# Performance work log

Measured on AMD Instinct MI355X. Metric: run time of the kernel, lower is better.

The kernel has to match this reference:

```python
import jax, jax.numpy as jnp
from jax import lax
import numpy as np

D_MODEL = 512
D_STATE = 16
D_CONV = 4
EXPAND = 2
D_INNER = EXPAND * D_MODEL  # 1024
DT_RANK = (D_MODEL + 15) // 16  # 32
FF_DIM = 1024
N_LAYERS = 2
B, L = 2, 2048


def setup_inputs() -> dict:
    key = jax.random.key(0)
    ks = jax.random.split(key, 16)
    s = 0.02
    x = jax.random.normal(ks[0], (B, L, D_MODEL), jnp.float32)
    in_proj_w = jax.random.normal(ks[1], (N_LAYERS, 2 * D_INNER, D_MODEL), jnp.float32) * s
    conv_w = jax.random.normal(ks[2], (N_LAYERS, D_INNER, D_CONV), jnp.float32) * 0.3
    conv_b = jax.random.normal(ks[3], (N_LAYERS, D_INNER), jnp.float32) * s
    x_proj_w = jax.random.normal(ks[4], (N_LAYERS, DT_RANK + 2 * D_STATE, D_INNER), jnp.float32) * s
    dt_proj_w = jax.random.normal(ks[5], (N_LAYERS, D_INNER, DT_RANK), jnp.float32) * s
    dt_proj_b = jax.random.normal(ks[6], (N_LAYERS, D_INNER), jnp.float32) * 0.5 - 4.0
    A_log = jnp.log(jnp.broadcast_to(jnp.arange(1, D_STATE + 1, dtype=jnp.float32), (N_LAYERS, D_INNER, D_STATE)))
    Dp = jnp.ones((N_LAYERS, D_INNER), jnp.float32)
    out_proj_w = jax.random.normal(ks[7], (N_LAYERS, D_MODEL, D_INNER), jnp.float32) * s
    mlp_w1 = jax.random.normal(ks[8], (FF_DIM, D_MODEL), jnp.float32) * s
    mlp_b1 = jnp.zeros((FF_DIM,), jnp.float32)
    mlp_w2 = jax.random.normal(ks[9], (D_MODEL, FF_DIM), jnp.float32) * s
    mlp_b2 = jnp.zeros((D_MODEL,), jnp.float32)
    return dict(x=x, in_proj_w=in_proj_w, conv_w=conv_w, conv_b=conv_b,
                x_proj_w=x_proj_w, dt_proj_w=dt_proj_w, dt_proj_b=dt_proj_b,
                A_log=A_log, Dp=Dp, out_proj_w=out_proj_w,
                mlp_w1=mlp_w1, mlp_b1=mlp_b1, mlp_w2=mlp_w2, mlp_b2=mlp_b2)


def _mamba_layer(x, ipw, cw, cb, xpw, dpw, dpb, Al, Dv, opw):
    # x: [B, L, d_model]
    b, l, _ = x.shape
    xz = jnp.einsum('bld,ed->ble', x, ipw)           # [B, L, 2*d_inner]
    xin, z = jnp.split(xz, 2, axis=-1)
    # causal depthwise conv1d (pad left d_conv-1)
    xc = jnp.transpose(xin, (0, 2, 1))               # [B, d_inner, L]
    xc = lax.conv_general_dilated(xc, cw[:, None, :], (1,), [(D_CONV - 1, 0)],
                                  feature_group_count=D_INNER)
    xin = jax.nn.silu(jnp.transpose(xc + cb[:, None], (0, 2, 1)))  # [B, L, d_inner]
    dbl = jnp.einsum('bld,ed->ble', xin, xpw)        # [B, L, dt_rank + 2*d_state]
    dt, Bm, Cm = jnp.split(dbl, [DT_RANK, DT_RANK + D_STATE], axis=-1)
    dt = jax.nn.softplus(jnp.einsum('blr,dr->bld', dt, dpw) + dpb)  # [B, L, d_inner]
    A = -jnp.exp(Al)                                  # [d_inner, d_state]
    dA = jnp.exp(dt[..., None] * A)                   # [B, L, d_inner, d_state]
    dBu = dt[..., None] * Bm[:, :, None, :] * xin[..., None]

    def step(h, inp):
        dA_t, dBu_t = inp
        h = dA_t * h + dBu_t
        return h, h

    h0 = jnp.zeros((b, D_INNER, D_STATE), x.dtype)
    _, hs = lax.scan(step, h0, (jnp.moveaxis(dA, 1, 0), jnp.moveaxis(dBu, 1, 0)))
    hs = jnp.moveaxis(hs, 0, 1)                       # [B, L, d_inner, d_state]
    y = jnp.einsum('blds,bls->bld', hs, Cm) + xin * Dv
    y = y * jax.nn.silu(z)
    return jnp.einsum('ble,de->bld', y, opw)


def reference(x, in_proj_w, conv_w, conv_b, x_proj_w, dt_proj_w, dt_proj_b,
              A_log, Dp, out_proj_w, mlp_w1, mlp_b1, mlp_w2, mlp_b2):
    residual = x
    for i in range(N_LAYERS):
        x = _mamba_layer(x, in_proj_w[i], conv_w[i], conv_b[i], x_proj_w[i],
                         dt_proj_w[i], dt_proj_b[i], A_log[i], Dp[i], out_proj_w[i])
    h = x + residual
    h = jax.nn.relu(jnp.einsum('bld,fd->blf', h, mlp_w1) + mlp_b1)  # dropout is identity in eval
    return jnp.einsum('blf,df->bld', h, mlp_w2) + mlp_b2
```

## Files before the change

kernel.cpp:

```cpp
#include <hip/hip_runtime.h>
#include <hip/hip_bf16.h>

#define BB 2
#define LL 2048
#define DMODEL 512
#define DSTATE 16
#define DINNER 1024
#define DTRANK 32
#define FFDIM 1024
#define MTOT (BB*LL)
#define SCL 64
#define NCC 32

typedef unsigned short u16;
typedef __attribute__((ext_vector_type(8))) short bf16x8;
typedef __attribute__((ext_vector_type(4))) float f32x4;

__device__ __forceinline__ float b2f(u16 u){
  unsigned v = ((unsigned)u) << 16; float f; __builtin_memcpy(&f, &v, 4); return f;
}
__device__ __forceinline__ u16 f2b(float f){
  unsigned u; __builtin_memcpy(&u, &f, 4);
  unsigned r = (u + 0x7FFFu + ((u >> 16) & 1u)) >> 16;
  return (u16)r;
}
__device__ __forceinline__ float siluf(float x){ return x / (1.f + __expf(-x)); }
__device__ __forceinline__ float softplusf(float v){
  return fmaxf(v, 0.f) + __logf(1.f + __expf(-fabsf(v)));
}

__device__ __forceinline__ float ldin(const void* p, size_t i, int bf){
  if (bf) return b2f(((const u16*)p)[i]);
  return ((const float*)p)[i];
}
__device__ __forceinline__ void stout(void* p, size_t i, int bf, float v){
  if (bf) ((u16*)p)[i] = f2b(v);
  else    ((float*)p)[i] = v;
}

__device__ __forceinline__ int getbf(const void* dp){
  return (*(const unsigned*)dp == 0x3F803F80u) ? 1 : 0;
}

template<int CVT>
__device__ __forceinline__ bf16x8 ld8(const void* P, size_t gi, int bf){
  if (!CVT || bf) return *(const bf16x8*)((const u16*)P + gi);
  float4 f0 = *(const float4*)((const float*)P + gi);
  float4 f1 = *(const float4*)((const float*)P + gi + 4);
  union { u16 u[8]; bf16x8 v; } t;
  t.u[0]=f2b(f0.x); t.u[1]=f2b(f0.y); t.u[2]=f2b(f0.z); t.u[3]=f2b(f0.w);
  t.u[4]=f2b(f1.x); t.u[5]=f2b(f1.y); t.u[6]=f2b(f1.z); t.u[7]=f2b(f1.w);
  return t.v;
}

#define CVT_IPW (2*2*DINNER*DMODEL)
#define CVT_XPW (2*64*DINNER)
#define CVT_DPW (2*DINNER*DTRANK)
#define CVT_OPW (2*DMODEL*DINNER)
#define CVT_W1  (FFDIM*DMODEL)
#define CVT_W2  (DMODEL*FFDIM)
#define CVT_CW  (2*DINNER*4)
#define CVT_CB  (2*DINNER)
#define CVT_TOT (CVT_IPW+CVT_XPW+CVT_DPW+CVT_OPW+CVT_W1+CVT_W2+CVT_CW+CVT_CB)
__global__ __launch_bounds__(256) void cvt_all_k(
    const void* __restrict__ ipw, const void* __restrict__ xpw,
    const void* __restrict__ dpw, const void* __restrict__ opw,
    const void* __restrict__ w1, const void* __restrict__ w2,
    const void* __restrict__ cw, const void* __restrict__ cb,
    u16* __restrict__ dst, const void* __restrict__ dprobe)
{
  const int bf = getbf(dprobe);
  size_t i4 = ((size_t)blockIdx.x * 256 + threadIdx.x) * 4;
  if (i4 >= CVT_TOT) return;
  const void* src; size_t off = i4;
  if      (off < CVT_IPW)                     { src = ipw; }
  else if ((off -= CVT_IPW) < CVT_XPW)        { src = xpw; }
  else if ((off -= CVT_XPW) < CVT_DPW)        { src = dpw; }
  else if ((off -= CVT_DPW) < CVT_OPW)        { src = opw; }
  else if ((off -= CVT_OPW) < CVT_W1)         { src = w1; }
  else if ((off -= CVT_W1)  < CVT_W2)         { src = w2; }
  else if ((off -= CVT_W2)  < CVT_CW)         { src = cw; }
  else     { off -= CVT_CW;                     src = cb; }
  ushort4 o;
  if (bf) {
    o = *(const ushort4*)((const u16*)src + off);
  } else {
    float4 f = *(const float4*)((const float*)src + off);
    o.x = f2b(f.x); o.y = f2b(f.y); o.z = f2b(f.z); o.w = f2b(f.w);
  }
  *(ushort4*)(dst + i4) = o;
}

template<int ACT, int CVA, int CVW, int CIN, int BM, int BN, int KB, int RESID>
__global__ __launch_bounds__(256) void gemm_mfma(
    const void* __restrict__ A, size_t aoff, int lda,
    const void* __restrict__ W, size_t woff,
    const void* __restrict__ bias, size_t boff,
    void* __restrict__ C, size_t coff, int ldc, int K,
    const void* __restrict__ xres, size_t xroff,
    const void* __restrict__ dprobe)
{
  const int bf = getbf(dprobe);
  constexpr int C8  = KB / 8;
  constexpr int TR  = 256 / C8;
  constexpr int ALD = BM / TR;
  constexpr int WLD = BN / TR;
  __shared__ __align__(16) u16 As[2][BM * KB];
  __shared__ __align__(16) u16 Ws[2][BN * KB];
  const int tid = threadIdx.x;
  const int row0 = blockIdx.y * BM, col0 = blockIdx.x * BN;
  const int wave = tid >> 6, lane = tid & 63;
  const int l15 = lane & 15, quad = lane >> 4;
  constexpr int WMT = (BM == 64) ? 1 : ((BN == 128) ? 4 : 2);
  const int mbase = (BM == 64) ? (wave * 16)
                  : ((BN == 128) ? (wave & 1) * 64 : wave * 32);
  const int nbase = (BM == 128 && BN == 128) ? (wave >> 1) * 64 : 0;

  const int rT = tid / C8, csw = tid % C8;
  const int scg = (KB == 32) ? (csw ^ ((rT >> 1) & 3)) : (csw ^ (rT & 7));
  const int lws = tid * 8;
  const size_t ab0 = aoff + (size_t)(row0 + rT) * lda + scg * 8;
  const size_t wb0 = woff + (size_t)(col0 + rT) * K   + scg * 8;

  f32x4 acc[WMT][4];
#pragma unroll
  for (int i = 0; i < WMT; i++)
#pragma unroll
    for (int j = 0; j < 4; j++) acc[i][j] = (f32x4){0.f,0.f,0.f,0.f};

  const int NT = K / KB;

  auto fchunk = [&](int r_, int g){
    return (KB == 32) ? (g ^ ((r_ >> 1) & 3)) : (g ^ (r_ & 7));
  };
  auto compute = [&](int cur_){
#pragma unroll
    for (int ks = 0; ks < KB / 32; ks++) {
      bf16x8 af_[WMT], bf_[4];
#pragma unroll
      for (int mt = 0; mt < WMT; mt++) {
        int r_ = mbase + mt * 16 + l15;
        af_[mt] = *(const bf16x8*)&As[cur_][r_ * KB + fchunk(r_, ks * 4 + quad) * 8];
      }
#pragma unroll
      for (int nt = 0; nt < 4; nt++) {
        int r_ = nbase + nt * 16 + l15;
        bf_[nt] = *(const bf16x8*)&Ws[cur_][r_ * KB + fchunk(r_, ks * 4 + quad) * 8];
      }
#pragma unroll
      for (int mt = 0; mt < WMT; mt++)
#pragma unroll
        for (int nt = 0; nt < 4; nt++)
          acc[mt][nt] = __builtin_amdgcn_mfma_f32_16x16x32_bf16(af_[mt], bf_[nt], acc[mt][nt], 0, 0, 0);
    }
  };

  bf16x8 ra0[ALD], rw0[WLD], ra1[ALD], rw1[WLD], ra2[ALD], rw2[WLD];

#define GLOAD(RA, RW, T) do { const int k1_ = (T) * KB;                        \
  _Pragma("unroll") for (int i = 0; i < ALD; i++)                              \
    RA[i] = ld8<CVA>(A, ab0 + k1_ + (size_t)i * TR * lda, bf);                 \
  _Pragma("unroll") for (int i = 0; i < WLD; i++)                              \
    RW[i] = ld8<CVW>(W, wb0 + k1_ + (size_t)i * TR * K, bf); } while (0)

#define GSTEP(RA, RW, T) do {                                                  \
  const int cur_ = (T) & 1;                                                    \
  _Pragma("unroll") for (int i = 0; i < ALD; i++)                              \
    *(bf16x8*)&As[cur_][lws + i * 2048] = RA[i];                               \
  _Pragma("unroll") for (int i = 0; i < WLD; i++)                              \
    *(bf16x8*)&Ws[cur_][lws + i * 2048] = RW[i];                               \
  if ((T) + 3 < NT) GLOAD(RA, RW, (T) + 3);                                    \
  __syncthreads();                                                             \
  compute(cur_);                                                               \
} while (0)

  GLOAD(ra0, rw0, 0);
  if (NT > 1) GLOAD(ra1, rw1, 1);
  if (NT > 2) GLOAD(ra2, rw2, 2);
  int t = 0;
  for (; t + 2 < NT; t += 3) {
    GSTEP(ra0, rw0, t);
    GSTEP(ra1, rw1, t + 1);
    GSTEP(ra2, rw2, t + 2);
  }
  if (t < NT)     GSTEP(ra0, rw0, t);
  if (t + 1 < NT) GSTEP(ra1, rw1, t + 1);
#undef GLOAD
#undef GSTEP

#pragma unroll
  for (int nt = 0; nt < 4; nt++) {
    int c = col0 + nbase + nt * 16 + l15;
    float bv = bias ? ldin(bias, boff + c, bf) : 0.f;
#pragma unroll
    for (int mt = 0; mt < WMT; mt++) {
      int rb = row0 + mbase + mt * 16 + quad * 4;
#pragma unroll
      for (int r = 0; r < 4; r++) {
        float v = acc[mt][nt][r] + bv;
        if (ACT == 1) v = softplusf(v);
        if (ACT == 2) v = fmaxf(v, 0.f);
        size_t ci = (size_t)(rb + r) * ldc + c;
        if (RESID) v += ldin(xres, xroff + ci, bf);
        if (CIN) stout(C, coff + ci, bf, v);
        else     ((u16*)C)[coff + ci] = f2b(v);
      }
    }
  }
}

template<int FST>
__global__ __launch_bounds__(256) void conv_k(
    const u16* __restrict__ xz, const void* __restrict__ cw, size_t cwo,
    const void* __restrict__ cb, size_t cbo, u16* __restrict__ xc,
    const void* __restrict__ dprobe)
{
  if (FST) {
    const u16* cw16 = (const u16*)cw;
    const u16* cb16 = (const u16*)cb;
    int idx8 = (blockIdx.x * 256 + threadIdx.x) * 8;
    int d8 = idx8 & 1023;
    int row = idx8 >> 10;
    int lb = row & (LL - 1);
    bf16x8 cwv0 = *(const bf16x8*)&cw16[cwo + d8*4];
    bf16x8 cwv1 = *(const bf16x8*)&cw16[cwo + d8*4 + 8];
    bf16x8 cwv2 = *(const bf16x8*)&cw16[cwo + d8*4 + 16];
    bf16x8 cwv3 = *(const bf16x8*)&cw16[cwo + d8*4 + 24];
    bf16x8 cbv  = *(const bf16x8*)&cb16[cbo + d8];
    bf16x8 xv0 = (bf16x8){0,0,0,0,0,0,0,0}, xv1 = xv0, xv2 = xv0, xv3 = xv0;
    if (lb >= 3) xv0 = *(const bf16x8*)&xz[(size_t)(row - 3) * 2048 + d8];
    if (lb >= 2) xv1 = *(const bf16x8*)&xz[(size_t)(row - 2) * 2048 + d8];
    if (lb >= 1) xv2 = *(const bf16x8*)&xz[(size_t)(row - 1) * 2048 + d8];
    xv3 = *(const bf16x8*)&xz[(size_t)row * 2048 + d8];
    bf16x8 ov;
#pragma unroll
    for (int i = 0; i < 8; i++) {
      float acc = b2f((u16)cbv[i]);
      int c0 = i * 4;
      float w0 = b2f((u16)((c0 < 8) ? cwv0[c0 & 7] : (c0 < 16) ? cwv1[c0 & 7] : (c0 < 24) ? cwv2[c0 & 7] : cwv3[c0 & 7]));
      float w1_ = b2f((u16)(((c0+1) < 8) ? cwv0[(c0+1) & 7] : ((c0+1) < 16) ? cwv1[(c0+1) & 7] : ((c0+1) < 24) ? cwv2[(c0+1) & 7] : cwv3[(c0+1) & 7]));
      float w2_ = b2f((u16)(((c0+2) < 8) ? cwv0[(c0+2) & 7] : ((c0+2) < 16) ? cwv1[(c0+2) & 7] : ((c0+2) < 24) ? cwv2[(c0+2) & 7] : cwv3[(c0+2) & 7]));
      float w3_ = b2f((u16)(((c0+3) < 8) ? cwv0[(c0+3) & 7] : ((c0+3) < 16) ? cwv1[(c0+3) & 7] : ((c0+3) < 24) ? cwv2[(c0+3) & 7] : cwv3[(c0+3) & 7]));
      acc += w0 * b2f((u16)xv0[i]);
      acc += w1_ * b2f((u16)xv1[i]);
      acc += w2_ * b2f((u16)xv2[i]);
      acc += w3_ * b2f((u16)xv3[i]);
      ov[i] = (short)f2b(siluf(acc));
    }
    *(bf16x8*)&xc[idx8] = ov;
  } else {
    const int bf = getbf(dprobe);
    int idx = blockIdx.x * 256 + threadIdx.x;
    int d = idx & 1023;
    int row = idx >> 10;
    int lb = row & (LL - 1);
    float acc = ldin(cb, cbo + d, bf);
#pragma unroll
    for (int k = 0; k < 4; k++) {
      int lk = lb - 3 + k;
      if (lk >= 0) acc += ldin(cw, cwo + d*4 + k, bf) * b2f(xz[(size_t)(row - 3 + k) * 2048 + d]);
    }
    xc[idx] = f2b(siluf(acc));
  }
}

template<int CVW>
__global__ __launch_bounds__(256) void scan_A_k(
    const u16* __restrict__ xc,
    const u16* __restrict__ dbl,
    const void* __restrict__ dpwp, size_t dpwo,
    const void* __restrict__ dpbp, size_t dpbo,
    const void* __restrict__ Alog, size_t alo,
    float* __restrict__ Pc, float* __restrict__ Sc,
    const void* __restrict__ dprobe)
{
  const int bf = getbf(dprobe);
  int bid = blockIdx.x;
  int b = bid >> 9;
  int c = (bid >> 4) & (NCC - 1);
  int g = bid & 15;
  int t = threadIdx.x;
  int dl = t >> 2, sq = t & 3;
  int d0 = g * 64, d = d0 + dl;
  int rowb = b * LL + c * SCL;

  __shared__ __align__(16) u16 dts[64 * 64];
  __shared__ __align__(16) u16 us[64 * 64];
  __shared__ __align__(16) float Bs[64 * 20];
  u16* dbls = dts;
  u16* dpws = dts + 64 * 32;

  {
    int r = t >> 2, c8 = (t & 3) * 8;
    *(bf16x8*)&dbls[r * 32 + c8] =
        *(const bf16x8*)&dbl[(size_t)(rowb + r) * 64 + c8];
    *(bf16x8*)&dpws[r * 32 + c8] =
        ld8<CVW>(dpwp, dpwo + (size_t)(d0 + r) * DTRANK + c8, bf);
  }
#pragma unroll
  for (int p = 0; p < 2; p++) {
    int seg = p * 256 + t;
    int r = seg >> 3, c8 = (seg & 7) * 8;
    bf16x8 uv = *(const bf16x8*)&xc[(size_t)(rowb + r) * 1024 + d0 + c8];
    int coff = r >> 3, roff = r & 7;
#pragma unroll
    for (int i = 0; i < 8; i++) {
      int dd = c8 + i;
      us[dd * 64 + ((coff ^ (dd & 7)) << 3) + roff] = (u16)uv[i];
    }
  }
  if (t < 128) {
    int l = t >> 1, grp = t & 1;
    bf16x8 v = *(const bf16x8*)&dbl[(size_t)(rowb + l) * 64 + 32 + grp * 8];
    f32x4 f0 = {b2f((u16)v[0]), b2f((u16)v[1]), b2f((u16)v[2]), b2f((u16)v[3])};
    f32x4 f1 = {b2f((u16)v[4]), b2f((u16)v[5]), b2f((u16)v[6]), b2f((u16)v[7])};
    *(f32x4*)&Bs[l * 20 + grp * 8]     = f0;
    *(f32x4*)&Bs[l * 20 + grp * 8 + 4] = f1;
  }
  float Av[4];
#pragma unroll
  for (int j = 0; j < 4; j++)
    Av[j] = -__expf(ldin(Alog, alo + (size_t)d * DSTATE + sq * 4 + j, bf));
  __syncthreads();

  {
    int wv = t >> 6, lane = t & 63;
    int fl = lane & 15, qd = lane >> 4;
    bf16x8 afr  = *(const bf16x8*)&dbls[(wv * 16 + fl) * 32 + qd * 8];
    bf16x8 bfr0 = *(const bf16x8*)&dpws[(fl)      * 32 + qd * 8];
    bf16x8 bfr1 = *(const bf16x8*)&dpws[(16 + fl) * 32 + qd * 8];
    bf16x8 bfr2 = *(const bf16x8*)&dpws[(32 + fl) * 32 + qd * 8];
    bf16x8 bfr3 = *(const bf16x8*)&dpws[(48 + fl) * 32 + qd * 8];
    __syncthreads();
    f32x4 zz = {0.f, 0.f, 0.f, 0.f};
    f32x4 a0 = __builtin_amdgcn_mfma_f32_16x16x32_bf16(afr, bfr0, zz, 0, 0, 0);
    f32x4 a1 = __builtin_amdgcn_mfma_f32_16x16x32_bf16(afr, bfr1, zz, 0, 0, 0);
    f32x4 a2 = __builtin_amdgcn_mfma_f32_16x16x32_bf16(afr, bfr2, zz, 0, 0, 0);
    f32x4 a3 = __builtin_amdgcn_mfma_f32_16x16x32_bf16(afr, bfr3, zz, 0, 0, 0);
    int lc = wv * 2 + (qd >> 1);
    int off = (qd & 1) * 4;
#define DTWR(AN, NT) do {                                                      \
    int dd_ = (NT) * 16 + fl;                                                  \
    float bvv_ = ldin(dpbp, dpbo + d0 + dd_, bf);                              \
    ushort4 pk_;                                                               \
    pk_.x = f2b(softplusf(AN[0] + bvv_));                                      \
    pk_.y = f2b(softplusf(AN[1] + bvv_));                                      \
    pk_.z = f2b(softplusf(AN[2] + bvv_));                                      \
    pk_.w = f2b(softplusf(AN[3] + bvv_));                                      \
    *(ushort4*)&dts[dd_ * 64 + ((lc ^ (dd_ & 7)) << 3) + off] = pk_; } while (0)
    DTWR(a0, 0); DTWR(a1, 1); DTWR(a2, 2); DTWR(a3, 3);
#undef DTWR
  }
  __syncthreads();

  float h[4] = {0.f,0.f,0.f,0.f}, P[4] = {1.f,1.f,1.f,1.f};
  for (int cc = 0; cc < 8; cc++) {
    int base = dl * 64 + ((cc ^ (dl & 7)) << 3);
    bf16x8 dt8 = *(const bf16x8*)&dts[base];
    bf16x8 u8  = *(const bf16x8*)&us[base];
#pragma unroll
    for (int i = 0; i < 8; i++) {
      int l = cc * 8 + i;
      float dtv = b2f((u16)dt8[i]);
      float uv  = b2f((u16)u8[i]);
      float dtu = dtv * uv;
      f32x4 B4 = *(const f32x4*)&Bs[l * 20 + sq * 4];
#pragma unroll
      for (int j = 0; j < 4; j++) {
        float dA = __expf(dtv * Av[j]);
        h[j] = dA * h[j] + dtu * B4[j];
        P[j] *= dA;
      }
    }
  }
  size_t o = (((size_t)b * DINNER + d) * NCC + c) * DSTATE + sq * 4;
  *(f32x4*)&Pc[o] = (f32x4){P[0], P[1], P[2], P[3]};
  *(f32x4*)&Sc[o] = (f32x4){h[0], h[1], h[2], h[3]};
}

__global__ __launch_bounds__(256) void scan_B_k(
    float* __restrict__ Pc, const float* __restrict__ Sc)
{
  int idx = blockIdx.x * 256 + threadIdx.x;
  int bd = idx >> 4, s = idx & 15;
  float h = 0.f;
  for (int c = 0; c < NCC; c++) {
    size_t o = ((size_t)bd * NCC + c) * DSTATE + s;
    float P = Pc[o], S = Sc[o];
    Pc[o] = h;
    h = P * h + S;
  }
}

template<int CVW>
__global__ __launch_bounds__(256) void scan_C_k(
    u16* __restrict__ dtp, int sdt, const u16* __restrict__ xz,
    const u16* __restrict__ xc,
    const u16* __restrict__ dbl,
    const void* __restrict__ dpwp, size_t dpwo,
    const void* __restrict__ dpbp, size_t dpbo,
    const void* __restrict__ Alog, size_t alo,
    const void* __restrict__ Dpt, size_t dpo, const float* __restrict__ Hinit,
    const void* __restrict__ dprobe)
{
  const int bf = getbf(dprobe);
  int bid = blockIdx.x;
  int b = bid >> 9;
  int c = (bid >> 4) & (NCC - 1);
  int g = bid & 15;
  int t = threadIdx.x;
  int dl = t >> 2, sq = t & 3;
  int d0 = g * 64, d = d0 + dl;
  int rowb = b * LL + c * SCL;

  __shared__ __align__(16) u16 dts[64 * 64];
  __shared__ __align__(16) u16 us[64 * 64];
  __shared__ __align__(16) u16 outs[64 * 64];
  __shared__ __align__(16) float BCs[64 * 36];
  u16* dbls = dts;
  u16* dpws = dts + 64 * 32;

  {
    int r = t >> 2, c8 = (t & 3) * 8;
    *(bf16x8*)&dbls[r * 32 + c8] =
        *(const bf16x8*)&dbl[(size_t)(rowb + r) * 64 + c8];
    *(bf16x8*)&dpws[r * 32 + c8] =
        ld8<CVW>(dpwp, dpwo + (size_t)(d0 + r) * DTRANK + c8, bf);
  }
#pragma unroll
  for (int p = 0; p < 2; p++) {
    int seg = p * 256 + t;
    int r = seg >> 3, c8 = (seg & 7) * 8;
    bf16x8 uv = *(const bf16x8*)&xc[(size_t)(rowb + r) * 1024 + d0 + c8];
    int coff = r >> 3, roff = r & 7;
#pragma unroll
    for (int i = 0; i < 8; i++) {
      int dd = c8 + i;
      us[dd * 64 + ((coff ^ (dd & 7)) << 3) + roff] = (u16)uv[i];
    }
  }
  {
    int l = t >> 2, grp = t & 3;
    bf16x8 v = *(const bf16x8*)&dbl[(size_t)(rowb + l) * 64 + 32 + grp * 8];
    f32x4 f0 = {b2f((u16)v[0]), b2f((u16)v[1]), b2f((u16)v[2]), b2f((u16)v[3])};
    f32x4 f1 = {b2f((u16)v[4]), b2f((u16)v[5]), b2f((u16)v[6]), b2f((u16)v[7])};
    *(f32x4*)&BCs[l * 36 + grp * 8]     = f0;
    *(f32x4*)&BCs[l * 36 + grp * 8 + 4] = f1;
  }
  float Av[4];
#pragma unroll
  for (int j = 0; j < 4; j++)
    Av[j] = -__expf(ldin(Alog, alo + (size_t)d * DSTATE + sq * 4 + j, bf));
  float Dv = ldin(Dpt, dpo + d, bf);
  float h[4];
  size_t o = (((size_t)b * DINNER + d) * NCC + c) * DSTATE + sq * 4;
  f32x4 h4 = *(const f32x4*)&Hinit[o];
  h[0] = h4[0]; h[1] = h4[1]; h[2] = h4[2]; h[3] = h4[3];
  __syncthreads();

  {
    int wv = t >> 6, lane = t & 63;
    int fl = lane & 15, qd = lane >> 4;
    bf16x8 afr  = *(const bf16x8*)&dbls[(wv * 16 + fl) * 32 + qd * 8];
    bf16x8 bfr0 = *(const bf16x8*)&dpws[(fl)      * 32 + qd * 8];
    bf16x8 bfr1 = *(const bf16x8*)&dpws[(16 + fl) * 32 + qd * 8];
    bf16x8 bfr2 = *(const bf16x8*)&dpws[(32 + fl) * 32 + qd * 8];
    bf16x8 bfr3 = *(const bf16x8*)&dpws[(48 + fl) * 32 + qd * 8];
    __syncthreads();
    f32x4 zz = {0.f, 0.f, 0.f, 0.f};
    f32x4 a0 = __builtin_amdgcn_mfma_f32_16x16x32_bf16(afr, bfr0, zz, 0, 0, 0);
    f32x4 a1 = __builtin_amdgcn_mfma_f32_16x16x32_bf16(afr, bfr1, zz, 0, 0, 0);
    f32x4 a2 = __builtin_amdgcn_mfma_f32_16x16x32_bf16(afr, bfr2, zz, 0, 0, 0);
    f32x4 a3 = __builtin_amdgcn_mfma_f32_16x16x32_bf16(afr, bfr3, zz, 0, 0, 0);
    int lc = wv * 2 + (qd >> 1);
    int off = (qd & 1) * 4;
#define DTWR(AN, NT) do {                                                      \
    int dd_ = (NT) * 16 + fl;                                                  \
    float bvv_ = ldin(dpbp, dpbo + d0 + dd_, bf);                              \
    ushort4 pk_;                                                               \
    pk_.x = f2b(softplusf(AN[0] + bvv_));                                      \
    pk_.y = f2b(softplusf(AN[1] + bvv_));                                      \
    pk_.z = f2b(softplusf(AN[2] + bvv_));                                      \
    pk_.w = f2b(softplusf(AN[3] + bvv_));                                      \
    *(ushort4*)&dts[dd_ * 64 + ((lc ^ (dd_ & 7)) << 3) + off] = pk_; } while (0)
    DTWR(a0, 0); DTWR(a1, 1); DTWR(a2, 2); DTWR(a3, 3);
#undef DTWR
  }
  __syncthreads();

  for (int cc = 0; cc < 8; cc++) {
    int base = dl * 64 + ((cc ^ (dl & 7)) << 3);
    bf16x8 dt8 = *(const bf16x8*)&dts[base];
    bf16x8 u8  = *(const bf16x8*)&us[base];
#pragma unroll
    for (int i = 0; i < 8; i++) {
      int l = cc * 8 + i;
      float dtv = b2f((u16)dt8[i]);
      float uv  = b2f((u16)u8[i]);
      float dtu = dtv * uv;
      f32x4 B4 = *(const f32x4*)&BCs[l * 36 + sq * 4];
      f32x4 C4 = *(const f32x4*)&BCs[l * 36 + 16 + sq * 4];
      float y = 0.f;
#pragma unroll
      for (int j = 0; j < 4; j++) {
        float dA = __expf(dtv * Av[j]);
        h[j] = dA * h[j] + dtu * B4[j];
        y += h[j] * C4[j];
      }
      y += __shfl_xor(y, 1);
      y += __shfl_xor(y, 2);
      if (sq == 0) outs[l * 64 + dl] = f2b(y + uv * Dv);
    }
  }
  __syncthreads();
#pragma unroll
  for (int p = 0; p < 2; p++) {
    int seg = p * 256 + t;
    int r = seg >> 3, c8 = (seg & 7) * 8;
    bf16x8 yv = *(const bf16x8*)&outs[r * 64 + c8];
    bf16x8 zv = *(const bf16x8*)&xz[(size_t)(rowb + r) * 2048 + 1024 + d0 + c8];
    bf16x8 ov;
#pragma unroll
    for (int i = 0; i < 8; i++) {
      float z = b2f((u16)zv[i]);
      ov[i] = (short)f2b(b2f((u16)yv[i]) * siluf(z));
    }
    *(bf16x8*)&dtp[(size_t)(rowb + r) * sdt + d0 + c8] = ov;
  }
}

extern "C" void kernel_launch(void* const* d_in, const int* in_sizes, int n_in,
                              void* d_out, int out_size, void* d_ws, size_t ws_size,
                              hipStream_t stream) {
  const void* x_in = d_in[0];
  const void* ipw  = d_in[1];
  const void* cw   = d_in[2];
  const void* cb   = d_in[3];
  const void* xpw  = d_in[4];
  const void* dpw  = d_in[5];
  const void* dpb  = d_in[6];
  const void* Alog = d_in[7];
  const void* Dpt  = d_in[8];
  const void* opw  = d_in[9];
  const void* w1   = d_in[10];
  const void* b1   = d_in[11];
  const void* w2   = d_in[12];
  const void* b2   = d_in[13];

  const bool full = ws_size >= (size_t)64 * 1024 * 1024;
  const bool bfh = (in_sizes[1] == (int)(CVT_IPW * 2));

  if (full) {
    float* Pc = (float*)((char*)d_ws + 64);
    float* Sc = Pc + (size_t)BB*DINNER*NCC*DSTATE;
    u16* p = (u16*)(Sc + (size_t)BB*DINNER*NCC*DSTATE);
    u16* cvt0  = p;
    u16* ipw16 = p;  p += (size_t)CVT_IPW;
    u16* xpw16 = p;  p += (size_t)CVT_XPW;
    u16* dpw16 = p;  p += (size_t)CVT_DPW;
    u16* opw16 = p;  p += (size_t)CVT_OPW;
    u16* w116  = p;  p += (size_t)CVT_W1;
    u16* w216  = p;  p += (size_t)CVT_W2;
    u16* cw16  = p;  p += (size_t)CVT_CW;
    u16* cb16  = p;  p += (size_t)CVT_CB;
    u16* xz    = p;  p += (size_t)MTOT*2*DINNER;
    u16* xc    = p;  p += (size_t)MTOT*DINNER;
    u16* dty   = p;  p += (size_t)MTOT*DINNER;
    u16* dbl   = p;
    u16* bx = xc;
    u16* resid = xz;
    u16* hid = xz + (size_t)4*1024*1024;

    const u16* Wipw = bfh ? (const u16*)ipw : ipw16;
    const u16* Wxpw = bfh ? (const u16*)xpw : xpw16;
    const u16* Wdpw = bfh ? (const u16*)dpw : dpw16;
    const u16* Wopw = bfh ? (const u16*)opw : opw16;
    const u16* Ww1  = bfh ? (const u16*)w1  : w116;
    const u16* Ww2  = bfh ? (const u16*)w2  : w216;
    const u16* Wcw  = bfh ? (const u16*)cw  : cw16;
    const u16* Wcb  = bfh ? (const u16*)cb  : cb16;
    if (!bfh)
      cvt_all_k<<<(CVT_TOT/4 + 255)/256, 256, 0, stream>>>(
          ipw, xpw, dpw, opw, w1, w2, cw, cb, cvt0, Dpt);

    for (int layer = 0; layer < 2; layer++) {
      size_t ipw_o = (size_t)layer*2*DINNER*DMODEL;
      size_t cw_o  = (size_t)layer*DINNER*4,  cb_o = (size_t)layer*DINNER;
      size_t xpw_o = (size_t)layer*64*DINNER, dpw_o = (size_t)layer*DINNER*DTRANK;
      size_t dpb_o = (size_t)layer*DINNER,    al_o = (size_t)layer*DINNER*DSTATE;
      size_t dp_o  = (size_t)layer*DINNER,    opw_o = (size_t)layer*DMODEL*DINNER;
      if (layer == 0)
        gemm_mfma<0,1,0,0,128,128,32,0><<<dim3(16, 32), 256, 0, stream>>>(
            x_in, 0, DMODEL, Wipw, ipw_o, nullptr, 0, xz, 0, 2048, DMODEL,
            nullptr, 0, Dpt);
      else
        gemm_mfma<0,0,0,0,128,128,32,0><<<dim3(16, 32), 256, 0, stream>>>(
            bx, 0, DMODEL, Wipw, ipw_o, nullptr, 0, xz, 0, 2048, DMODEL,
            nullptr, 0, Dpt);
      conv_k<1><<<MTOT*DINNER/2048, 256, 0, stream>>>(
          xz, Wcw, cw_o, Wcb, cb_o, xc, Dpt);
      gemm_mfma<0,0,0,0,64,64,32,0><<<dim3(1, 64), 256, 0, stream>>>(
          xc, 0, DINNER, Wxpw, xpw_o, nullptr, 0, dbl, 0, 64, DINNER,
          nullptr, 0, Dpt);
      scan_A_k<0><<<BB*NCC*16, 256, 0, stream>>>(
          xc, dbl, Wdpw, dpw_o, dpb, dpb_o, Alog, al_o, Pc, Sc, Dpt);
      scan_B_k<<<BB*64, 256, 0, stream>>>(Pc, Sc);
      scan_C_k<0><<<BB*NCC*16, 256, 0, stream>>>(
          dty, 1024, xz, xc, dbl, Wdpw, dpw_o, dpb, dpb_o, Alog, al_o,
          Dpt, dp_o, Pc, Dpt);
      if (layer == 0)
        gemm_mfma<0,0,0,0,64,64,32,0><<<dim3(8, 64), 256, 0, stream>>>(
            dty, 0, 1024, Wopw, opw_o, nullptr, 0, bx, 0, DMODEL, DINNER,
            nullptr, 0, Dpt);
      else
        gemm_mfma<0,0,0,0,64,64,32,1><<<dim3(8, 64), 256, 0, stream>>>(
            dty, 0, 1024, Wopw, opw_o, nullptr, 0, resid, 0, DMODEL, DINNER,
            x_in, 0, Dpt);
    }
    gemm_mfma<2,0,0,0,64,64,32,0><<<dim3(16, 64), 256, 0, stream>>>(
        resid, 0, DMODEL, Ww1, 0, b1, 0, hid, 0, FFDIM, DMODEL,
        nullptr, 0, Dpt);
    gemm_mfma<0,0,0,1,64,64,32,0><<<dim3(8, 64), 256, 0, stream>>>(
        hid, 0, FFDIM, Ww2, 0, b2, 0, d_out, 0, DMODEL, FFDIM,
        nullptr, 0, Dpt);
  } else {
    float* Pc = (float*)((char*)d_ws + 64);
    float* Sc = Pc + (size_t)DINNER*NCC*DSTATE;
    u16* p = (u16*)(Sc + (size_t)DINNER*NCC*DSTATE);
    u16* xz  = p;  p += (size_t)LL*2*DINNER;
    u16* xc  = p;  p += (size_t)LL*DINNER;
    u16* bxF = p;  p += (size_t)MTOT*DMODEL;
    u16* dbl = p;
    u16* hid = xz + (size_t)2*1024*1024;

    for (int layer = 0; layer < 2; layer++) {
      size_t ipw_o = (size_t)layer*2*DINNER*DMODEL;
      size_t cw_o  = (size_t)layer*DINNER*4,  cb_o = (size_t)layer*DINNER;
      size_t xpw_o = (size_t)layer*64*DINNER, dpw_o = (size_t)layer*DINNER*DTRANK;
      size_t dpb_o = (size_t)layer*DINNER,    al_o = (size_t)layer*DINNER*DSTATE;
      size_t dp_o  = (size_t)layer*DINNER,    opw_o = (size_t)layer*DMODEL*DINNER;
      for (int b = 0; b < BB; b++) {
        size_t ro = (size_t)b * LL * DMODEL;
        if (layer == 0)
          gemm_mfma<0,1,1,0,128,128,32,0><<<dim3(16, 16), 256, 0, stream>>>(
              x_in, ro, DMODEL, ipw, ipw_o, nullptr, 0, xz, 0, 2048, DMODEL,
              nullptr, 0, Dpt);
        else
          gemm_mfma<0,0,1,0,128,128,32,0><<<dim3(16, 16), 256, 0, stream>>>(
              bxF, ro, DMODEL, ipw, ipw_o, nullptr, 0, xz, 0, 2048, DMODEL,
              nullptr, 0, Dpt);
        conv_k<0><<<LL*DINNER/256, 256, 0, stream>>>(xz, cw, cw_o, cb, cb_o, xc, Dpt);
        gemm_mfma<0,0,1,0,64,64,32,0><<<dim3(1, 32), 256, 0, stream>>>(
            xc, 0, DINNER, xpw, xpw_o, nullptr, 0, dbl, 0, 64, DINNER,
            nullptr, 0, Dpt);
        scan_A_k<1><<<NCC*16, 256, 0, stream>>>(
            xc, dbl, dpw, dpw_o, dpb, dpb_o, Alog, al_o, Pc, Sc, Dpt);
        scan_B_k<<<64, 256, 0, stream>>>(Pc, Sc);
        scan_C_k<1><<<NCC*16, 256, 0, stream>>>(
            xz, 2048, xz, xc, dbl, dpw, dpw_o, dpb, dpb_o, Alog, al_o,
            Dpt, dp_o, Pc, Dpt);
        if (layer == 0)
          gemm_mfma<0,0,1,0,64,64,32,0><<<dim3(8, 32), 256, 0, stream>>>(
              xz, 0, 2048, opw, opw_o, nullptr, 0, bxF, ro, DMODEL, DINNER,
              nullptr, 0, Dpt);
        else
          gemm_mfma<0,0,1,0,64,64,32,1><<<dim3(8, 32), 256, 0, stream>>>(
              xz, 0, 2048, opw, opw_o, nullptr, 0, bxF, ro, DMODEL, DINNER,
              x_in, ro, Dpt);
      }
    }
    for (int b = 0; b < BB; b++) {
      size_t ro = (size_t)b * LL * DMODEL;
      gemm_mfma<2,0,1,0,64,64,32,0><<<dim3(16, 32), 256, 0, stream>>>(
          bxF, ro, DMODEL, w1, 0, b1, 0, hid, 0, FFDIM, DMODEL,
          nullptr, 0, Dpt);
      gemm_mfma<0,0,1,1,64,64,32,0><<<dim3(8, 32), 256, 0, stream>>>(
          hid, 0, FFDIM, w2, 0, b2, 0, d_out, ro, DMODEL, FFDIM,
          nullptr, 0, Dpt);
    }
  }
}
```

Measured before the change: 331.9 us.

## Fuse chunked scan passes into one cooperative kernel with grid syncs

Replaces the three scan launches (chunk-local scan, cross-chunk prefix, and output pass) with one cooperative kernel that uses two grid-wide syncs. The delta and u tiles stay in shared memory across the passes, so the second pass no longer reloads them or recomputes the dt projection. It also removes two kernel launches. The cost is that all 1024 blocks must be co-resident at 4 blocks per CU under the launch bounds, and two grid barriers are added. If the cooperative launch fails, the code falls back to the old three kernels.

```diff
diff --git a/kernel.cpp b/kernel.cpp
--- a/kernel.cpp
+++ b/kernel.cpp
@@ -1,5 +1,8 @@
 #include <hip/hip_runtime.h>
 #include <hip/hip_bf16.h>
+#include <hip/hip_cooperative_groups.h>
+
+namespace cg = cooperative_groups;
 
 #define BB 2
 #define LL 2048
@@ -264,13 +267,13 @@
   }
 }
 
-template<int CVW>
-__global__ __launch_bounds__(256) void scan_A_k(
-    const u16* __restrict__ xc,
-    const u16* __restrict__ dbl,
+__global__ __launch_bounds__(256, 4) void scan_fused_k(
+    u16* __restrict__ dtp, int sdt, const u16* __restrict__ xz,
+    const u16* __restrict__ xc, const u16* __restrict__ dbl,
     const void* __restrict__ dpwp, size_t dpwo,
     const void* __restrict__ dpbp, size_t dpbo,
     const void* __restrict__ Alog, size_t alo,
+    const void* __restrict__ Dpt, size_t dpo,
     float* __restrict__ Pc, float* __restrict__ Sc,
     const void* __restrict__ dprobe)
 {
@@ -286,7 +289,8 @@
 
   __shared__ __align__(16) u16 dts[64 * 64];
   __shared__ __align__(16) u16 us[64 * 64];
-  __shared__ __align__(16) float Bs[64 * 20];
+  __shared__ __align__(16) u16 outs[64 * 64];
+  __shared__ __align__(16) float BCs[64 * 36];
   u16* dbls = dts;
   u16* dpws = dts + 64 * 32;
 
@@ -295,7 +299,7 @@
     *(bf16x8*)&dbls[r * 32 + c8] =
         *(const bf16x8*)&dbl[(size_t)(rowb + r) * 64 + c8];
     *(bf16x8*)&dpws[r * 32 + c8] =
-        ld8<CVW>(dpwp, dpwo + (size_t)(d0 + r) * DTRANK + c8, bf);
+        ld8<0>(dpwp, dpwo + (size_t)(d0 + r) * DTRANK + c8, bf);
   }
 #pragma unroll
   for (int p = 0; p < 2; p++) {
@@ -309,18 +313,19 @@
       us[dd * 64 + ((coff ^ (dd & 7)) << 3) + roff] = (u16)uv[i];
     }
   }
-  if (t < 128) {
-    int l = t >> 1, grp = t & 1;
+  {
+    int l = t >> 2, grp = t & 3;
     bf16x8 v = *(const bf16x8*)&dbl[(size_t)(rowb + l) * 64 + 32 + grp * 8];
     f32x4 f0 = {b2f((u16)v[0]), b2f((u16)v[1]), b2f((u16)v[2]), b2f((u16)v[3])};
     f32x4 f1 = {b2f((u16)v[4]), b2f((u16)v[5]), b2f((u16)v[6]), b2f((u16)v[7])};
-    *(f32x4*)&Bs[l * 20 + grp * 8]     = f0;
-    *(f32x4*)&Bs[l * 20 + grp * 8 + 4] = f1;
+    *(f32x4*)&BCs[l * 36 + grp * 8]     = f0;
+    *(f32x4*)&BCs[l * 36 + grp * 8 + 4] = f1;
   }
   float Av[4];
 #pragma unroll
   for (int j = 0; j < 4; j++)
     Av[j] = -__expf(ldin(Alog, alo + (size_t)d * DSTATE + sq * 4 + j, bf));
+  float Dv = ldin(Dpt, dpo + d, bf);
   __syncthreads();
 
   {
@@ -353,7 +358,54 @@
   }
   __syncthreads();
 
-  float h[4] = {0.f,0.f,0.f,0.f}, P[4] = {1.f,1.f,1.f,1.f};
+  size_t o = (((size_t)b * DINNER + d) * NCC + c) * DSTATE + sq * 4;
+
+  {
+    float h[4] = {0.f,0.f,0.f,0.f}, P[4] = {1.f,1.f,1.f,1.f};
+    for (int cc = 0; cc < 8; cc++) {
+      int base = dl * 64 + ((cc ^ (dl & 7)) << 3);
+      bf16x8 dt8 = *(const bf16x8*)&dts[base];
+      bf16x8 u8  = *(const bf16x8*)&us[base];
+#pragma unroll
+      for (int i = 0; i < 8; i++) {
+        int l = cc * 8 + i;
+        float dtv = b2f((u16)dt8[i]);
+        float uv  = b2f((u16)u8[i]);
+        float dtu = dtv * uv;
+        f32x4 B4 = *(const f32x4*)&BCs[l * 36 + sq * 4];
+#pragma unroll
+        for (int j = 0; j < 4; j++) {
+          float dA = __expf(dtv * Av[j]);
+          h[j] = dA * h[j] + dtu * B4[j];
+          P[j] *= dA;
+        }
+      }
+    }
+    *(f32x4*)&Pc[o] = (f32x4){P[0], P[1], P[2], P[3]};
+    *(f32x4*)&Sc[o] = (f32x4){h[0], h[1], h[2], h[3]};
+  }
+
+  cg::this_grid().sync();
+
+  if (bid < BB * 64) {
+    int idx = bid * 256 + t;
+    int bd = idx >> 4, s = idx & 15;
+    float hh = 0.f;
+    for (int c2 = 0; c2 < NCC; c2++) {
+      size_t o2 = ((size_t)bd * NCC + c2) * DSTATE + s;
+      float Pv = Pc[o2], Sv = Sc[o2];
+      Pc[o2] = hh;
+      hh = Pv * hh + Sv;
+    }
+  }
+
+  cg::this_grid().sync();
+
+  float h[4];
+  {
+    f32x4 h4 = *(const f32x4*)&Pc[o];
+    h[0] = h4[0]; h[1] = h4[1]; h[2] = h4[2]; h[3] = h4[3];
+  }
   for (int cc = 0; cc < 8; cc++) {
     int base = dl * 64 + ((cc ^ (dl & 7)) << 3);
     bf16x8 dt8 = *(const bf16x8*)&dts[base];
@@ -364,43 +416,45 @@
       float dtv = b2f((u16)dt8[i]);
       float uv  = b2f((u16)u8[i]);
       float dtu = dtv * uv;
-      f32x4 B4 = *(const f32x4*)&Bs[l * 20 + sq * 4];
+      f32x4 B4 = *(const f32x4*)&BCs[l * 36 + sq * 4];
+      f32x4 C4 = *(const f32x4*)&BCs[l * 36 + 16 + sq * 4];
+      float y = 0.f;
 #pragma unroll
       for (int j = 0; j < 4; j++) {
         float dA = __expf(dtv * Av[j]);
         h[j] = dA * h[j] + dtu * B4[j];
-        P[j] *= dA;
+        y += h[j] * C4[j];
       }
-    }
-  }
-  size_t o = (((size_t)b * DINNER + d) * NCC + c) * DSTATE + sq * 4;
-  *(f32x4*)&Pc[o] = (f32x4){P[0], P[1], P[2], P[3]};
-  *(f32x4*)&Sc[o] = (f32x4){h[0], h[1], h[2], h[3]};
-}
-
-__global__ __launch_bounds__(256) void scan_B_k(
-    float* __restrict__ Pc, const float* __restrict__ Sc)
-{
-  int idx = blockIdx.x * 256 + threadIdx.x;
-  int bd = idx >> 4, s = idx & 15;
-  float h = 0.f;
-  for (int c = 0; c < NCC; c++) {
-    size_t o = ((size_t)bd * NCC + c) * DSTATE + s;
-    float P = Pc[o], S = Sc[o];
-    Pc[o] = h;
-    h = P * h + S;
+      y += __shfl_xor(y, 1);
+      y += __shfl_xor(y, 2);
+      if (sq == 0) outs[l * 64 + dl] = f2b(y + uv * Dv);
+    }
+  }
+  __syncthreads();
+#pragma unroll
+  for (int p = 0; p < 2; p++) {
+    int seg = p * 256 + t;
+    int r = seg >> 3, c8 = (seg & 7) * 8;
+    bf16x8 yv = *(const bf16x8*)&outs[r * 64 + c8];
+    bf16x8 zv = *(const bf16x8*)&xz[(size_t)(rowb + r) * 2048 + 1024 + d0 + c8];
+    bf16x8 ov;
+#pragma unroll
+    for (int i = 0; i < 8; i++) {
+      float z = b2f((u16)zv[i]);
+      ov[i] = (short)f2b(b2f((u16)yv[i]) * siluf(z));
+    }
+    *(bf16x8*)&dtp[(size_t)(rowb + r) * sdt + d0 + c8] = ov;
   }
 }
 
 template<int CVW>
-__global__ __launch_bounds__(256) void scan_C_k(
-    u16* __restrict__ dtp, int sdt, const u16* __restrict__ xz,
+__global__ __launch_bounds__(256) void scan_A_k(
     const u16* __restrict__ xc,
     const u16* __restrict__ dbl,
     const void* __restrict__ dpwp, size_t dpwo,
     const void* __restrict__ dpbp, size_t dpbo,
     const void* __restrict__ Alog, size_t alo,
-    const void* __restrict__ Dpt, size_t dpo, const float* __restrict__ Hinit,
+    float* __restrict__ Pc, float* __restrict__ Sc,
     const void* __restrict__ dprobe)
 {
   const int bf = getbf(dprobe);
@@ -415,8 +469,7 @@
 
   __shared__ __align__(16) u16 dts[64 * 64];
   __shared__ __align__(16) u16 us[64 * 64];
-  __shared__ __align__(16) u16 outs[64 * 64];
-  __shared__ __align__(16) float BCs[64 * 36];
+  __shared__ __align__(16) float Bs[64 * 20];
   u16* dbls = dts;
   u16* dpws = dts + 64 * 32;
 
@@ -439,23 +492,18 @@
       us[dd * 64 + ((coff ^ (dd & 7)) << 3) + roff] = (u16)uv[i];
     }
   }
-  {
-    int l = t >> 2, grp = t & 3;
+  if (t < 128) {
+    int l = t >> 1, grp = t & 1;
     bf16x8 v = *(const bf16x8*)&dbl[(size_t)(rowb + l) * 64 + 32 + grp * 8];
     f32x4 f0 = {b2f((u16)v[0]), b2f((u16)v[1]), b2f((u16)v[2]), b2f((u16)v[3])};
     f32x4 f1 = {b2f((u16)v[4]), b2f((u16)v[5]), b2f((u16)v[6]), b2f((u16)v[7])};
-    *(f32x4*)&BCs[l * 36 + grp * 8]     = f0;
-    *(f32x4*)&BCs[l * 36 + grp * 8 + 4] = f1;
+    *(f32x4*)&Bs[l * 20 + grp * 8]     = f0;
+    *(f32x4*)&Bs[l * 20 + grp * 8 + 4] = f1;
   }
   float Av[4];
 #pragma unroll
   for (int j = 0; j < 4; j++)
     Av[j] = -__expf(ldin(Alog, alo + (size_t)d * DSTATE + sq * 4 + j, bf));
-  float Dv = ldin(Dpt, dpo + d, bf);
-  float h[4];
-  size_t o = (((size_t)b * DINNER + d) * NCC + c) * DSTATE + sq * 4;
-  f32x4 h4 = *(const f32x4*)&Hinit[o];
-  h[0] = h4[0]; h[1] = h4[1]; h[2] = h4[2]; h[3] = h4[3];
   __syncthreads();
 
   {
@@ -488,6 +536,141 @@
   }
   __syncthreads();
 
+  float h[4] = {0.f,0.f,0.f,0.f}, P[4] = {1.f,1.f,1.f,1.f};
+  for (int cc = 0; cc < 8; cc++) {
+    int base = dl * 64 + ((cc ^ (dl & 7)) << 3);
+    bf16x8 dt8 = *(const bf16x8*)&dts[base];
+    bf16x8 u8  = *(const bf16x8*)&us[base];
+#pragma unroll
+    for (int i = 0; i < 8; i++) {
+      int l = cc * 8 + i;
+      float dtv = b2f((u16)dt8[i]);
+      float uv  = b2f((u16)u8[i]);
+      float dtu = dtv * uv;
+      f32x4 B4 = *(const f32x4*)&Bs[l * 20 + sq * 4];
+#pragma unroll
+      for (int j = 0; j < 4; j++) {
+        float dA = __expf(dtv * Av[j]);
+        h[j] = dA * h[j] + dtu * B4[j];
+        P[j] *= dA;
+      }
+    }
+  }
+  size_t o = (((size_t)b * DINNER + d) * NCC + c) * DSTATE + sq * 4;
+  *(f32x4*)&Pc[o] = (f32x4){P[0], P[1], P[2], P[3]};
+  *(f32x4*)&Sc[o] = (f32x4){h[0], h[1], h[2], h[3]};
+}
+
+__global__ __launch_bounds__(256) void scan_B_k(
+    float* __restrict__ Pc, const float* __restrict__ Sc)
+{
+  int idx = blockIdx.x * 256 + threadIdx.x;
+  int bd = idx >> 4, s = idx & 15;
+  float h = 0.f;
+  for (int c = 0; c < NCC; c++) {
+    size_t o = ((size_t)bd * NCC + c) * DSTATE + s;
+    float P = Pc[o], S = Sc[o];
+    Pc[o] = h;
+    h = P * h + S;
+  }
+}
+
+template<int CVW>
+__global__ __launch_bounds__(256) void scan_C_k(
+    u16* __restrict__ dtp, int sdt, const u16* __restrict__ xz,
+    const u16* __restrict__ xc,
+    const u16* __restrict__ dbl,
+    const void* __restrict__ dpwp, size_t dpwo,
+    const void* __restrict__ dpbp, size_t dpbo,
+    const void* __restrict__ Alog, size_t alo,
+    const void* __restrict__ Dpt, size_t dpo, const float* __restrict__ Hinit,
+    const void* __restrict__ dprobe)
+{
+  const int bf = getbf(dprobe);
+  int bid = blockIdx.x;
+  int b = bid >> 9;
+  int c = (bid >> 4) & (NCC - 1);
+  int g = bid & 15;
+  int t = threadIdx.x;
+  int dl = t >> 2, sq = t & 3;
+  int d0 = g * 64, d = d0 + dl;
+  int rowb = b * LL + c * SCL;
+
+  __shared__ __align__(16) u16 dts[64 * 64];
+  __shared__ __align__(16) u16 us[64 * 64];
+  __shared__ __align__(16) u16 outs[64 * 64];
+  __shared__ __align__(16) float BCs[64 * 36];
+  u16* dbls = dts;
+  u16* dpws = dts + 64 * 32;
+
+  {
+    int r = t >> 2, c8 = (t & 3) * 8;
+    *(bf16x8*)&dbls[r * 32 + c8] =
+        *(const bf16x8*)&dbl[(size_t)(rowb + r) * 64 + c8];
+    *(bf16x8*)&dpws[r * 32 + c8] =
+        ld8<CVW>(dpwp, dpwo + (size_t)(d0 + r) * DTRANK + c8, bf);
+  }
+#pragma unroll
+  for (int p = 0; p < 2; p++) {
+    int seg = p * 256 + t;
+    int r = seg >> 3, c8 = (seg & 7) * 8;
+    bf16x8 uv = *(const bf16x8*)&xc[(size_t)(rowb + r) * 1024 + d0 + c8];
+    int coff = r >> 3, roff = r & 7;
+#pragma unroll
+    for (int i = 0; i < 8; i++) {
+      int dd = c8 + i;
+      us[dd * 64 + ((coff ^ (dd & 7)) << 3) + roff] = (u16)uv[i];
+    }
+  }
+  {
+    int l = t >> 2, grp = t & 3;
+    bf16x8 v = *(const bf16x8*)&dbl[(size_t)(rowb + l) * 64 + 32 + grp * 8];
+    f32x4 f0 = {b2f((u16)v[0]), b2f((u16)v[1]), b2f((u16)v[2]), b2f((u16)v[3])};
+    f32x4 f1 = {b2f((u16)v[4]), b2f((u16)v[5]), b2f((u16)v[6]), b2f((u16)v[7])};
+    *(f32x4*)&BCs[l * 36 + grp * 8]     = f0;
+    *(f32x4*)&BCs[l * 36 + grp * 8 + 4] = f1;
+  }
+  float Av[4];
+#pragma unroll
+  for (int j = 0; j < 4; j++)
+    Av[j] = -__expf(ldin(Alog, alo + (size_t)d * DSTATE + sq * 4 + j, bf));
+  float Dv = ldin(Dpt, dpo + d, bf);
+  float h[4];
+  size_t o = (((size_t)b * DINNER + d) * NCC + c) * DSTATE + sq * 4;
+  f32x4 h4 = *(const f32x4*)&Hinit[o];
+  h[0] = h4[0]; h[1] = h4[1]; h[2] = h4[2]; h[3] = h4[3];
+  __syncthreads();
+
+  {
+    int wv = t >> 6, lane = t & 63;
+    int fl = lane & 15, qd = lane >> 4;
+    bf16x8 afr  = *(const bf16x8*)&dbls[(wv * 16 + fl) * 32 + qd * 8];
+    bf16x8 bfr0 = *(const bf16x8*)&dpws[(fl)      * 32 + qd * 8];
+    bf16x8 bfr1 = *(const bf16x8*)&dpws[(16 + fl) * 32 + qd * 8];
+    bf16x8 bfr2 = *(const bf16x8*)&dpws[(32 + fl) * 32 + qd * 8];
+    bf16x8 bfr3 = *(const bf16x8*)&dpws[(48 + fl) * 32 + qd * 8];
+    __syncthreads();
+    f32x4 zz = {0.f, 0.f, 0.f, 0.f};
+    f32x4 a0 = __builtin_amdgcn_mfma_f32_16x16x32_bf16(afr, bfr0, zz, 0, 0, 0);
+    f32x4 a1 = __builtin_amdgcn_mfma_f32_16x16x32_bf16(afr, bfr1, zz, 0, 0, 0);
+    f32x4 a2 = __builtin_amdgcn_mfma_f32_16x16x32_bf16(afr, bfr2, zz, 0, 0, 0);
+    f32x4 a3 = __builtin_amdgcn_mfma_f32_16x16x32_bf16(afr, bfr3, zz, 0, 0, 0);
+    int lc = wv * 2 + (qd >> 1);
+    int off = (qd & 1) * 4;
+#define DTWR(AN, NT) do {                                                      \
+    int dd_ = (NT) * 16 + fl;                                                  \
+    float bvv_ = ldin(dpbp, dpbo + d0 + dd_, bf);                              \
+    ushort4 pk_;                                                               \
+    pk_.x = f2b(softplusf(AN[0] + bvv_));                                      \
+    pk_.y = f2b(softplusf(AN[1] + bvv_));                                      \
+    pk_.z = f2b(softplusf(AN[2] + bvv_));                                      \
+    pk_.w = f2b(softplusf(AN[3] + bvv_));                                      \
+    *(ushort4*)&dts[dd_ * 64 + ((lc ^ (dd_ & 7)) << 3) + off] = pk_; } while (0)
+    DTWR(a0, 0); DTWR(a1, 1); DTWR(a2, 2); DTWR(a3, 3);
+#undef DTWR
+  }
+  __syncthreads();
+
   for (int cc = 0; cc < 8; cc++) {
     int base = dl * 64 + ((cc ^ (dl & 7)) << 3);
     bf16x8 dt8 = *(const bf16x8*)&dts[base];
@@ -602,12 +785,30 @@
       gemm_mfma<0,0,0,0,64,64,32,0><<<dim3(1, 64), 256, 0, stream>>>(
           xc, 0, DINNER, Wxpw, xpw_o, nullptr, 0, dbl, 0, 64, DINNER,
           nullptr, 0, Dpt);
-      scan_A_k<0><<<BB*NCC*16, 256, 0, stream>>>(
-          xc, dbl, Wdpw, dpw_o, dpb, dpb_o, Alog, al_o, Pc, Sc, Dpt);
-      scan_B_k<<<BB*64, 256, 0, stream>>>(Pc, Sc);
-      scan_C_k<0><<<BB*NCC*16, 256, 0, stream>>>(
-          dty, 1024, xz, xc, dbl, Wdpw, dpw_o, dpb, dpb_o, Alog, al_o,
-          Dpt, dp_o, Pc, Dpt);
+      {
+        u16* dtp_ = dty; int sdt_ = 1024;
+        const u16* xz_ = xz; const u16* xc_ = xc; const u16* dbl_ = dbl;
+        const void* dpw_ = Wdpw; size_t dpwo_ = dpw_o;
+        const void* dpb_ = dpb;  size_t dpbo_ = dpb_o;
+        const void* al_  = Alog; size_t alo_  = al_o;
+        const void* dp_  = Dpt;  size_t dpo_  = dp_o;
+        float* Pc_ = Pc; float* Sc_ = Sc;
+        const void* probe_ = Dpt;
+        void* sargs[] = {&dtp_, &sdt_, &xz_, &xc_, &dbl_, &dpw_, &dpwo_,
+                         &dpb_, &dpbo_, &al_, &alo_, &dp_, &dpo_,
+                         &Pc_, &Sc_, &probe_};
+        hipError_t ce = hipLaunchCooperativeKernel(
+            reinterpret_cast<void*>(scan_fused_k),
+            dim3(BB*NCC*16), dim3(256), sargs, 0, stream);
+        if (ce != hipSuccess) {
+          scan_A_k<0><<<BB*NCC*16, 256, 0, stream>>>(
+              xc, dbl, Wdpw, dpw_o, dpb, dpb_o, Alog, al_o, Pc, Sc, Dpt);
+          scan_B_k<<<BB*64, 256, 0, stream>>>(Pc, Sc);
+          scan_C_k<0><<<BB*NCC*16, 256, 0, stream>>>(
+              dty, 1024, xz, xc, dbl, Wdpw, dpw_o, dpb, dpb_o, Alog, al_o,
+              Dpt, dp_o, Pc, Dpt);
+        }
+      }
       if (layer == 0)
         gemm_mfma<0,0,0,0,64,64,32,0><<<dim3(8, 64), 256, 0, stream>>>(
             dty, 0, 1024, Wopw, opw_o, nullptr, 0, bx, 0, DMODEL, DINNER,
```

Measured after the change: 736.3 us. 122% more time.
